# Performance work log

Measured on AMD Instinct MI355X. Metric: run time of the kernel, lower is better.

Reference implementation:

```python
import jax, jax.numpy as jnp
import numpy as np

INF = 1.0e10


def _embed(x, W1, b1, W2, b2):
    # TemplateAngleEmbedder: Linear -> GELU -> Linear
    return jax.nn.gelu(x @ W1 + b1) @ W2 + b2


def setup_inputs() -> dict:
    key = jax.random.key(0)
    ks = jax.random.split(key, 12)
    B, N, K = 2, 768, 30
    d_pair, d_msa, relpos_k = 128, 256, 32
    num_bins = 2 * relpos_k + 1  # 65
    s = 0.02
    # valid rigid frames: random rotations via QR (det fixed to +1) + translations
    A = jax.random.normal(ks[0], (B, N, 3, 3), dtype=jnp.float32)
    Q, _ = jnp.linalg.qr(A)
    Q = Q * jnp.sign(jnp.linalg.det(Q))[..., None, None]
    t = jax.random.normal(ks[1], (B, N, 3), dtype=jnp.float32) * 10.0
    frames = (jnp.zeros((B, N, 4, 4), dtype=jnp.float32)
              .at[..., :3, :3].set(Q)
              .at[..., :3, 3].set(t)
              .at[..., 3, 3].set(1.0))
    residue_index = jnp.tile(jnp.arange(N, dtype=jnp.int32)[None], (B, 1))
    return {
        'tf': jax.random.normal(ks[2], (B, N, 1), dtype=jnp.float32),
        'residue_index': residue_index,
        'true_frame_tensor': frames,
        'seq_mask': jnp.ones((B, N), dtype=jnp.float32),
        'W_tf': jax.random.normal(ks[3], (1, d_msa), dtype=jnp.float32) * s,
        'b_tf': jnp.zeros((d_msa,), dtype=jnp.float32),
        'Wa1': jax.random.normal(ks[4], (5, d_pair), dtype=jnp.float32) * s,
        'ba1': jnp.zeros((d_pair,), dtype=jnp.float32),
        'Wa2': jax.random.normal(ks[5], (d_pair, d_pair), dtype=jnp.float32) * s,
        'ba2': jnp.zeros((d_pair,), dtype=jnp.float32),
        'Wd1': jax.random.normal(ks[6], (3, d_pair), dtype=jnp.float32) * s,
        'bd1': jnp.zeros((d_pair,), dtype=jnp.float32),
        'Wd2': jax.random.normal(ks[7], (d_pair, d_pair), dtype=jnp.float32) * s,
        'bd2': jnp.zeros((d_pair,), dtype=jnp.float32),
        'W_rp': jax.random.normal(ks[8], (num_bins, d_pair), dtype=jnp.float32) * s,
        'b_rp': jnp.zeros((d_pair,), dtype=jnp.float32),
        'topk': 30,
    }


def _pair_features(true_frame_tensor, residue_index, seq_mask, topk):
    # get_pair_info: pairwise dist + masked topk KNN + gather + frame decompose
    B, N = residue_index.shape
    R = true_frame_tensor[..., :3, :3]          # [B,N,3,3]
    t = true_frame_tensor[..., :3, 3]           # [B,N,3]
    xyz = t[:, None, :, :] - t[:, :, None, :]   # [B,i,j,3] = t_j - t_i
    dist = jnp.linalg.norm(xyz, axis=-1)        # [B,N,N]
    eye = jnp.eye(N, dtype=bool)[None]          # [1,N,N]
    smask = seq_mask.astype(bool)
    pair_mask = smask[:, None, :] & smask[:, :, None]
    rel = residue_index[:, None, :] - residue_index[:, :, None]
    connect = jnp.abs(rel) == 1
    d4topk = jnp.where(eye, INF, dist)
    d4topk = jnp.where(pair_mask, d4topk, INF)
    d4topk = jnp.where(connect, -INF, d4topk)
    _, idx = jax.lax.top_k(-d4topk, topk)       # k smallest -> [B,N,K]
    topk_dist = jnp.take_along_axis(dist, idx, axis=-1)          # [B,N,K]
    knn_mask = jnp.take_along_axis(pair_mask & ~eye, idx, axis=-1)
    # gather neighbor frames and decompose into frame i's local coordinates:
    # t_rel = R_i^T (t_j - t_i)
    bidx = jnp.arange(B)[:, None, None]
    tj = t[bidx, idx]                            # [B,N,K,3]
    t_rel = jnp.einsum('bnxy,bnkx->bnky', R, tj - t[:, :, None, :])
    d = topk_dist[..., None]
    direct_angle = jnp.where(d > 0, t_rel / jnp.where(d > 0, d, 1.0), 0.0)
    eye_g = jnp.take_along_axis(jnp.broadcast_to(eye, (B, N, N)), idx, axis=-1)
    conn_g = jnp.take_along_axis(connect, idx, axis=-1)
    f32 = topk_dist.dtype
    ang_in = jnp.concatenate([eye_g[..., None].astype(f32),
                              conn_g[..., None].astype(f32),
                              direct_angle], axis=-1)            # [B,N,K,5]
    dst_in = jnp.concatenate([eye_g[..., None].astype(f32),
                              conn_g[..., None].astype(f32),
                              topk_dist[..., None]], axis=-1)    # [B,N,K,3]
    return ang_in, dst_in, knn_mask


def reference(tf, residue_index, true_frame_tensor, seq_mask,
              W_tf, b_tf, Wa1, ba1, Wa2, ba2, Wd1, bd1, Wd2, bd2,
              W_rp, b_rp, topk):
    relpos_k = (W_rp.shape[0] - 1) // 2
    # pair info computed under no_grad in the original
    ang_in, dst_in, _ = jax.lax.stop_gradient(
        _pair_features(true_frame_tensor, residue_index, seq_mask, topk))
    # tf is replaced by ones in the original forward
    ones_tf = jnp.ones_like(tf[..., :1])
    s = ones_tf @ W_tf + b_tf                                   # [B,N,d_msa]
    pair_rep_angle = _embed(ang_in, Wa1, ba1, Wa2, ba2)         # [B,N,K,d_pair]
    pair_rep_dist = _embed(dst_in, Wd1, bd1, Wd2, bd2)          # [B,N,K,d_pair]
    # relpos embedding (use_chain_relative=False)
    rp = residue_index[:, :, None] - residue_index[:, None, :]
    rp = jnp.clip(rp, -relpos_k, relpos_k) + relpos_k
    oh = jax.nn.one_hot(rp, W_rp.shape[0], dtype=W_rp.dtype)    # [B,N,N,65]
    relpos_emb = oh @ W_rp + b_rp                               # [B,N,N,d_pair]
    return (s, pair_rep_angle, pair_rep_dist, relpos_emb)
```

## Files before the change

### kernel.cpp

```cpp
#include <hip/hip_runtime.h>

typedef unsigned short u16;
typedef unsigned int   u32;
typedef unsigned long long u64;

typedef __attribute__((ext_vector_type(8))) short  short8;
typedef __attribute__((ext_vector_type(4))) float  floatx4;

__device__ __forceinline__ u16 f2bf(float f) {
    u32 u = __float_as_uint(f);
    u32 r = (u + 0x7FFFu + ((u >> 16) & 1u)) >> 16;
    return (u16)r;
}
__device__ __forceinline__ float bfu2f(u16 u) {
    union { u32 i; float f; } v; v.i = ((u32)u) << 16; return v.f;
}

constexpr int N     = 768;
constexpr int TOPK  = 30;
constexpr long OFF_ANG = 393216;
constexpr long OFF_DST = 6291456;
constexpr long OFF_RP  = 12189696;

__device__ __forceinline__ float dist_f32(float dx, float dy, float dz) {
    float s = __fadd_rn(__fadd_rn(__fmul_rn(dx, dx), __fmul_rn(dy, dy)), __fmul_rn(dz, dz));
    return __fsqrt_rn(s);
}

__global__ __launch_bounds__(256) void topk_feat_kernel(
    const float* __restrict__ frames, const int* __restrict__ resi,
    const float* __restrict__ smask, float* __restrict__ feat)
{
    __shared__ float s_t[N * 3];
    __shared__ float s_m[N];
    __shared__ int   s_r[N];
    int tid = threadIdx.x;
    int r0  = blockIdx.x * 4;
    int b   = r0 / N;
    for (int j = tid; j < N; j += 256) {
        s_r[j] = resi[b * N + j];
        s_m[j] = smask[b * N + j];
        long fb = (long)(b * N + j) * 16;
        s_t[j * 3 + 0] = frames[fb + 0 * 4 + 3];
        s_t[j * 3 + 1] = frames[fb + 1 * 4 + 3];
        s_t[j * 3 + 2] = frames[fb + 2 * 4 + 3];
    }
    __syncthreads();

    int wave = tid >> 6, lane = tid & 63;
    int r = r0 + wave;
    int i = r - b * N;
    float ti0 = s_t[i * 3], ti1 = s_t[i * 3 + 1], ti2 = s_t[i * 3 + 2];
    float mi = s_m[i];
    int   ri = s_r[i];

    u64 keys[12];
#pragma unroll
    for (int c = 0; c < 12; c++) {
        int j = lane + 64 * c;
        float dx = __fadd_rn(s_t[j * 3 + 0], -ti0);
        float dy = __fadd_rn(s_t[j * 3 + 1], -ti1);
        float dz = __fadd_rn(s_t[j * 3 + 2], -ti2);
        float dist = dist_f32(dx, dy, dz);
        int rd = s_r[j] - ri;
        bool conn = (rd == 1) || (rd == -1);
        bool bad  = (j == i) || (mi == 0.f) || (s_m[j] == 0.f);
        float d4 = conn ? -1e10f : (bad ? 1e10f : dist);
        u32 u = __float_as_uint(d4);
        u32 su = (u >> 31) ? ~u : (u | 0x80000000u);
        keys[c] = ((u64)su << 32) | (u32)j;
    }

    int my_j = 0;
    for (int k = 0; k < TOPK; k++) {
        u64 m = keys[0];
#pragma unroll
        for (int c = 1; c < 12; c++) m = m < keys[c] ? m : keys[c];
#pragma unroll
        for (int off = 32; off >= 1; off >>= 1) {
            u32 lo = (u32)m, hi = (u32)(m >> 32);
            u32 lo2 = __shfl_xor(lo, off);
            u32 hi2 = __shfl_xor(hi, off);
            u64 o = ((u64)hi2 << 32) | lo2;
            m = m < o ? m : o;
        }
#pragma unroll
        for (int c = 0; c < 12; c++) keys[c] = (keys[c] == m) ? ~0ull : keys[c];
        if (lane == k) my_j = (int)(m & 0xffffffffu);
    }

    if (lane < TOPK) {
        int j = my_j;
        float dx = __fadd_rn(s_t[j * 3 + 0], -ti0);
        float dy = __fadd_rn(s_t[j * 3 + 1], -ti1);
        float dz = __fadd_rn(s_t[j * 3 + 2], -ti2);
        float dist = dist_f32(dx, dy, dz);
        long fb = (long)(b * N + i) * 16;
        float R00 = frames[fb + 0], R01 = frames[fb + 1], R02 = frames[fb + 2];
        float R10 = frames[fb + 4], R11 = frames[fb + 5], R12 = frames[fb + 6];
        float R20 = frames[fb + 8], R21 = frames[fb + 9], R22 = frames[fb + 10];
        float t0 = R00 * dx + R10 * dy + R20 * dz;
        float t1 = R01 * dx + R11 * dy + R21 * dz;
        float t2 = R02 * dx + R12 * dy + R22 * dz;
        float a0 = dist > 0.f ? t0 / dist : 0.f;
        float a1 = dist > 0.f ? t1 / dist : 0.f;
        float a2 = dist > 0.f ? t2 / dist : 0.f;
        int rd = s_r[j] - ri;
        float conn = ((rd == 1) || (rd == -1)) ? 1.f : 0.f;
        float eye  = (j == i) ? 1.f : 0.f;
        long base = ((long)r * TOPK + lane) * 8;
        feat[base + 0] = eye; feat[base + 1] = conn;
        feat[base + 2] = a0;  feat[base + 3] = a1; feat[base + 4] = a2;
        feat[base + 5] = eye; feat[base + 6] = conn; feat[base + 7] = dist;
    }
}

template<int NF, int FOFF>
__device__ __forceinline__ void embed_body3(
    int blk0, const float* __restrict__ feat,
    const float* __restrict__ W1, const float* __restrict__ b1,
    const float* __restrict__ W2, const float* __restrict__ b2,
    float* __restrict__ out,
    u16* s_w2h, u16* s_w2l, float* s_w1, float* s_b1, float* s_b2)
{
    int tid = threadIdx.x;
    for (int e4 = tid; e4 < 4096; e4 += 256) {
        floatx4 w4 = ((const floatx4*)W2)[e4];
        int e  = e4 * 4;
        int kk = e >> 7, nn0 = e & 127;
#pragma unroll
        for (int x = 0; x < 4; x++) {
            float w  = w4[x];
            u16 hi = f2bf(w);
            float lo = __fadd_rn(w, -bfu2f(hi));
            s_w2h[(nn0 + x) * 136 + kk] = hi;
            s_w2l[(nn0 + x) * 136 + kk] = f2bf(lo);
        }
    }
    for (int e = tid; e < NF * 128; e += 256) s_w1[e] = W1[e];
    if (tid < 128) { s_b1[tid] = b1[tid]; s_b2[tid] = b2[tid]; }
    __syncthreads();

    int wave = tid >> 6, lane = tid & 63;
    int m = lane & 15, q = lane >> 4;

#pragma unroll
    for (int tt = 0; tt < 3; tt++) {
        int blk  = blk0 + 240 * tt;
        int row0 = blk * 64 + wave * 16;
        int row  = row0 + m;

        float f[NF];
#pragma unroll
        for (int t = 0; t < NF; t++) f[t] = feat[(long)row * 8 + FOFF + t];

        floatx4 acc[8];
#pragma unroll
        for (int nt = 0; nt < 8; nt++) acc[nt] = (floatx4){0.f, 0.f, 0.f, 0.f};

#pragma unroll
        for (int s = 0; s < 4; s++) {
            short8 ahi, alo;
#pragma unroll
            for (int jj = 0; jj < 8; jj++) {
                int kk = 32 * s + 8 * q + jj;
                float h = s_b1[kk];
#pragma unroll
                for (int t = 0; t < NF; t++) h += f[t] * s_w1[t * 128 + kk];
                float u  = 0.7978845608028654f * (h + 0.044715f * h * h * h);
                float e2 = __expf(-2.f * fabsf(u));
                float th = (1.f - e2) / (1.f + e2);
                th = u < 0.f ? -th : th;
                float g = 0.5f * h * (1.f + th);
                u16 ghi = f2bf(g);
                float glo = __fadd_rn(g, -bfu2f(ghi));
                ahi[jj] = (short)ghi;
                alo[jj] = (short)f2bf(glo);
            }
#pragma unroll
            for (int nt = 0; nt < 8; nt++) {
                int boff = (nt * 16 + m) * 136 + 32 * s + 8 * q;
                short8 bh = *(const short8*)&s_w2h[boff];
                short8 bl = *(const short8*)&s_w2l[boff];
                acc[nt] = __builtin_amdgcn_mfma_f32_16x16x32_bf16(ahi, bh, acc[nt], 0, 0, 0);
                acc[nt] = __builtin_amdgcn_mfma_f32_16x16x32_bf16(alo, bh, acc[nt], 0, 0, 0);
                acc[nt] = __builtin_amdgcn_mfma_f32_16x16x32_bf16(ahi, bl, acc[nt], 0, 0, 0);
            }
        }

#pragma unroll
        for (int nt = 0; nt < 8; nt++) {
#pragma unroll
            for (int rg = 0; rg < 4; rg++) {
                int rr = row0 + q * 4 + rg;
                int cc = nt * 16 + m;
                out[(long)rr * 128 + cc] = acc[nt][rg] + s_b2[cc];
            }
        }
    }
}

__global__ __launch_bounds__(256) void mega_kernel(
    const int* __restrict__ resi,
    const float* __restrict__ W_rp, const float* __restrict__ b_rp,
    const float* __restrict__ feat,
    const float* __restrict__ Wa1, const float* __restrict__ ba1,
    const float* __restrict__ Wa2, const float* __restrict__ ba2,
    const float* __restrict__ Wd1, const float* __restrict__ bd1,
    const float* __restrict__ Wd2, const float* __restrict__ bd2,
    const float* __restrict__ W_tf, const float* __restrict__ b_tf,
    float* __restrict__ out)
{
    __shared__ __align__(16) char smem_raw[73216];
    int tid = threadIdx.x;
    unsigned bx = blockIdx.x;

    if (bx < 1152) {
        float* T   = (float*)smem_raw;
        int*   s_r = (int*)(T + 65 * 128);

        int blk = bx;
        int b   = blk >= 576;

        for (int e = tid; e < 65 * 128; e += 256) T[e] = W_rp[e] + b_rp[e & 127];
        for (int j = tid; j < N; j += 256) s_r[j] = resi[b * N + j];
        __syncthreads();

        long vbase   = (long)blk << 15;
        int  rowbase = (blk - b * 576) << 10;
        floatx4* dst = (floatx4*)(out + OFF_RP) + vbase;

#pragma unroll 4
        for (int it = 0; it < 128; ++it) {
            int lv  = (it << 8) + tid;
            unsigned lrow = (unsigned)(rowbase + (lv >> 5));
            int seg = lv & 31;
            unsigned i = lrow / 768u;
            unsigned j = lrow - i * 768u;
            int d = s_r[i] - s_r[j];
            d = d < -32 ? -32 : (d > 32 ? 32 : d);
            dst[lv] = ((const floatx4*)(T + (unsigned)(d + 32) * 128))[seg];
        }
    } else if (bx < 1632) {
        u16*   s_w2h = (u16*)smem_raw;
        u16*   s_w2l = (u16*)(smem_raw + 34816);
        float* s_w1  = (float*)(smem_raw + 69632);
        float* s_b1  = (float*)(smem_raw + 72192);
        float* s_b2  = (float*)(smem_raw + 72704);
        unsigned eb = bx - 1152;
        if (eb < 240) {
            embed_body3<5, 0>(eb, feat, Wa1, ba1, Wa2, ba2, out + OFF_ANG,
                              s_w2h, s_w2l, s_w1, s_b1, s_b2);
        } else {
            embed_body3<3, 5>(eb - 240, feat, Wd1, bd1, Wd2, bd2, out + OFF_DST,
                              s_w2h, s_w2l, s_w1, s_b1, s_b2);
        }
    } else {
        int gid = (bx - 1632) * 256 + tid;
        int c0  = (gid * 4) & 255;
        floatx4 o;
        o.x = W_tf[c0 + 0] + b_tf[c0 + 0];
        o.y = W_tf[c0 + 1] + b_tf[c0 + 1];
        o.z = W_tf[c0 + 2] + b_tf[c0 + 2];
        o.w = W_tf[c0 + 3] + b_tf[c0 + 3];
        *((floatx4*)out + gid) = o;
    }
}

extern "C" void kernel_launch(void* const* d_in, const int* in_sizes, int n_in,
                              void* d_out, int out_size, void* d_ws, size_t ws_size,
                              hipStream_t stream) {
    const int*   resi   = (const int*)d_in[1];
    const float* frames = (const float*)d_in[2];
    const float* smask  = (const float*)d_in[3];
    const float* W_tf   = (const float*)d_in[4];
    const float* b_tf   = (const float*)d_in[5];
    const float* Wa1    = (const float*)d_in[6];
    const float* ba1    = (const float*)d_in[7];
    const float* Wa2    = (const float*)d_in[8];
    const float* ba2    = (const float*)d_in[9];
    const float* Wd1    = (const float*)d_in[10];
    const float* bd1    = (const float*)d_in[11];
    const float* Wd2    = (const float*)d_in[12];
    const float* bd2    = (const float*)d_in[13];
    const float* W_rp   = (const float*)d_in[14];
    const float* b_rp   = (const float*)d_in[15];
    float* out  = (float*)d_out;
    float* feat = (float*)d_ws;

    hipLaunchKernelGGL(topk_feat_kernel, dim3(384), dim3(256), 0, stream,
                       frames, resi, smask, feat);
    hipLaunchKernelGGL(mega_kernel, dim3(2016), dim3(256), 0, stream,
                       resi, W_rp, b_rp, feat,
                       Wa1, ba1, Wa2, ba2, Wd1, bd1, Wd2, bd2,
                       W_tf, b_tf, out);
}
```

Measured before the change: 747.5 us.

## Pre-split W2 into bf16 hi/lo in global memory and shrink mega-kernel LDS

The bf16 hi/lo split and transpose of the second-layer weights moves out of every embed block into two extra blocks of the top-k kernel, which write it to workspace. Embed blocks now read those B fragments straight from global/L2 instead of LDS, and each block handles one 64-row tile instead of three. Shared memory drops to the relpos table size and launch bounds ask for 4 blocks per CU, which should raise occupancy for the memory-bound relpos writes. The cost is repeated global loads of the weight fragments inside the MFMA loop and more embed blocks that each reload W1 and biases.

```diff
diff --git a/kernel.cpp b/kernel.cpp
--- a/kernel.cpp
+++ b/kernel.cpp
@@ -27,14 +27,37 @@
     return __fsqrt_rn(s);
 }
 
-__global__ __launch_bounds__(256) void topk_feat_kernel(
+__global__ __launch_bounds__(256) void topk_feat_split_kernel(
     const float* __restrict__ frames, const int* __restrict__ resi,
-    const float* __restrict__ smask, float* __restrict__ feat)
+    const float* __restrict__ smask,
+    const float* __restrict__ Wa2, const float* __restrict__ Wd2,
+    float* __restrict__ feat, u16* __restrict__ w2sp)
 {
     __shared__ float s_t[N * 3];
     __shared__ float s_m[N];
     __shared__ int   s_r[N];
     int tid = threadIdx.x;
+
+    if (blockIdx.x >= 384) {
+        const float* W2 = (blockIdx.x == 384) ? Wa2 : Wd2;
+        u16* h = w2sp + (blockIdx.x - 384) * 32768;
+        u16* l = h + 16384;
+        for (int e4 = tid; e4 < 4096; e4 += 256) {
+            floatx4 w4 = ((const floatx4*)W2)[e4];
+            int e  = e4 * 4;
+            int kk = e >> 7, nn0 = e & 127;
+#pragma unroll
+            for (int x = 0; x < 4; x++) {
+                float w  = w4[x];
+                u16 hi = f2bf(w);
+                float lo = __fadd_rn(w, -bfu2f(hi));
+                h[(nn0 + x) * 128 + kk] = hi;
+                l[(nn0 + x) * 128 + kk] = f2bf(lo);
+            }
+        }
+        return;
+    }
+
     int r0  = blockIdx.x * 4;
     int b   = r0 / N;
     for (int j = tid; j < N; j += 256) {
@@ -116,102 +139,85 @@
 }
 
 template<int NF, int FOFF>
-__device__ __forceinline__ void embed_body3(
-    int blk0, const float* __restrict__ feat,
+__device__ __forceinline__ void embed_g(
+    int blk, const float* __restrict__ feat,
     const float* __restrict__ W1, const float* __restrict__ b1,
-    const float* __restrict__ W2, const float* __restrict__ b2,
+    const u16* __restrict__ w2h, const u16* __restrict__ w2l,
+    const float* __restrict__ b2,
     float* __restrict__ out,
-    u16* s_w2h, u16* s_w2l, float* s_w1, float* s_b1, float* s_b2)
+    float* s_w1, float* s_b1, float* s_b2)
 {
     int tid = threadIdx.x;
-    for (int e4 = tid; e4 < 4096; e4 += 256) {
-        floatx4 w4 = ((const floatx4*)W2)[e4];
-        int e  = e4 * 4;
-        int kk = e >> 7, nn0 = e & 127;
-#pragma unroll
-        for (int x = 0; x < 4; x++) {
-            float w  = w4[x];
-            u16 hi = f2bf(w);
-            float lo = __fadd_rn(w, -bfu2f(hi));
-            s_w2h[(nn0 + x) * 136 + kk] = hi;
-            s_w2l[(nn0 + x) * 136 + kk] = f2bf(lo);
-        }
-    }
     for (int e = tid; e < NF * 128; e += 256) s_w1[e] = W1[e];
     if (tid < 128) { s_b1[tid] = b1[tid]; s_b2[tid] = b2[tid]; }
     __syncthreads();
 
     int wave = tid >> 6, lane = tid & 63;
     int m = lane & 15, q = lane >> 4;
-
-#pragma unroll
-    for (int tt = 0; tt < 3; tt++) {
-        int blk  = blk0 + 240 * tt;
-        int row0 = blk * 64 + wave * 16;
-        int row  = row0 + m;
-
-        float f[NF];
-#pragma unroll
-        for (int t = 0; t < NF; t++) f[t] = feat[(long)row * 8 + FOFF + t];
-
-        floatx4 acc[8];
-#pragma unroll
-        for (int nt = 0; nt < 8; nt++) acc[nt] = (floatx4){0.f, 0.f, 0.f, 0.f};
-
-#pragma unroll
-        for (int s = 0; s < 4; s++) {
-            short8 ahi, alo;
-#pragma unroll
-            for (int jj = 0; jj < 8; jj++) {
-                int kk = 32 * s + 8 * q + jj;
-                float h = s_b1[kk];
-#pragma unroll
-                for (int t = 0; t < NF; t++) h += f[t] * s_w1[t * 128 + kk];
-                float u  = 0.7978845608028654f * (h + 0.044715f * h * h * h);
-                float e2 = __expf(-2.f * fabsf(u));
-                float th = (1.f - e2) / (1.f + e2);
-                th = u < 0.f ? -th : th;
-                float g = 0.5f * h * (1.f + th);
-                u16 ghi = f2bf(g);
-                float glo = __fadd_rn(g, -bfu2f(ghi));
-                ahi[jj] = (short)ghi;
-                alo[jj] = (short)f2bf(glo);
-            }
-#pragma unroll
-            for (int nt = 0; nt < 8; nt++) {
-                int boff = (nt * 16 + m) * 136 + 32 * s + 8 * q;
-                short8 bh = *(const short8*)&s_w2h[boff];
-                short8 bl = *(const short8*)&s_w2l[boff];
-                acc[nt] = __builtin_amdgcn_mfma_f32_16x16x32_bf16(ahi, bh, acc[nt], 0, 0, 0);
-                acc[nt] = __builtin_amdgcn_mfma_f32_16x16x32_bf16(alo, bh, acc[nt], 0, 0, 0);
-                acc[nt] = __builtin_amdgcn_mfma_f32_16x16x32_bf16(ahi, bl, acc[nt], 0, 0, 0);
-            }
-        }
-
+    int row0 = blk * 64 + wave * 16;
+    int row  = row0 + m;
+
+    float f[NF];
+#pragma unroll
+    for (int t = 0; t < NF; t++) f[t] = feat[(long)row * 8 + FOFF + t];
+
+    floatx4 acc[8];
+#pragma unroll
+    for (int nt = 0; nt < 8; nt++) acc[nt] = (floatx4){0.f, 0.f, 0.f, 0.f};
+
+#pragma unroll
+    for (int s = 0; s < 4; s++) {
+        short8 ahi, alo;
+#pragma unroll
+        for (int jj = 0; jj < 8; jj++) {
+            int kk = 32 * s + 8 * q + jj;
+            float h = s_b1[kk];
+#pragma unroll
+            for (int t = 0; t < NF; t++) h += f[t] * s_w1[t * 128 + kk];
+            float u  = 0.7978845608028654f * (h + 0.044715f * h * h * h);
+            float e2 = __expf(-2.f * fabsf(u));
+            float th = (1.f - e2) / (1.f + e2);
+            th = u < 0.f ? -th : th;
+            float g = 0.5f * h * (1.f + th);
+            u16 ghi = f2bf(g);
+            float glo = __fadd_rn(g, -bfu2f(ghi));
+            ahi[jj] = (short)ghi;
+            alo[jj] = (short)f2bf(glo);
+        }
 #pragma unroll
         for (int nt = 0; nt < 8; nt++) {
-#pragma unroll
-            for (int rg = 0; rg < 4; rg++) {
-                int rr = row0 + q * 4 + rg;
-                int cc = nt * 16 + m;
-                out[(long)rr * 128 + cc] = acc[nt][rg] + s_b2[cc];
-            }
-        }
-    }
-}
-
-__global__ __launch_bounds__(256) void mega_kernel(
+            int boff = (nt * 16 + m) * 128 + 32 * s + 8 * q;
+            short8 bh = *(const short8*)&w2h[boff];
+            short8 bl = *(const short8*)&w2l[boff];
+            acc[nt] = __builtin_amdgcn_mfma_f32_16x16x32_bf16(ahi, bh, acc[nt], 0, 0, 0);
+            acc[nt] = __builtin_amdgcn_mfma_f32_16x16x32_bf16(alo, bh, acc[nt], 0, 0, 0);
+            acc[nt] = __builtin_amdgcn_mfma_f32_16x16x32_bf16(ahi, bl, acc[nt], 0, 0, 0);
+        }
+    }
+
+#pragma unroll
+    for (int nt = 0; nt < 8; nt++) {
+#pragma unroll
+        for (int rg = 0; rg < 4; rg++) {
+            int rr = row0 + q * 4 + rg;
+            int cc = nt * 16 + m;
+            out[(long)rr * 128 + cc] = acc[nt][rg] + s_b2[cc];
+        }
+    }
+}
+
+__global__ __launch_bounds__(256, 4) void mega_kernel(
     const int* __restrict__ resi,
     const float* __restrict__ W_rp, const float* __restrict__ b_rp,
-    const float* __restrict__ feat,
+    const float* __restrict__ feat, const u16* __restrict__ w2sp,
     const float* __restrict__ Wa1, const float* __restrict__ ba1,
-    const float* __restrict__ Wa2, const float* __restrict__ ba2,
+    const float* __restrict__ ba2,
     const float* __restrict__ Wd1, const float* __restrict__ bd1,
-    const float* __restrict__ Wd2, const float* __restrict__ bd2,
+    const float* __restrict__ bd2,
     const float* __restrict__ W_tf, const float* __restrict__ b_tf,
     float* __restrict__ out)
 {
-    __shared__ __align__(16) char smem_raw[73216];
+    __shared__ __align__(16) char smem_raw[65 * 128 * 4 + N * 4];
     int tid = threadIdx.x;
     unsigned bx = blockIdx.x;
 
@@ -241,22 +247,22 @@
             d = d < -32 ? -32 : (d > 32 ? 32 : d);
             dst[lv] = ((const floatx4*)(T + (unsigned)(d + 32) * 128))[seg];
         }
-    } else if (bx < 1632) {
-        u16*   s_w2h = (u16*)smem_raw;
-        u16*   s_w2l = (u16*)(smem_raw + 34816);
-        float* s_w1  = (float*)(smem_raw + 69632);
-        float* s_b1  = (float*)(smem_raw + 72192);
-        float* s_b2  = (float*)(smem_raw + 72704);
+    } else if (bx < 2592) {
+        float* s_w1 = (float*)smem_raw;
+        float* s_b1 = (float*)(smem_raw + 2560);
+        float* s_b2 = (float*)(smem_raw + 3072);
         unsigned eb = bx - 1152;
-        if (eb < 240) {
-            embed_body3<5, 0>(eb, feat, Wa1, ba1, Wa2, ba2, out + OFF_ANG,
-                              s_w2h, s_w2l, s_w1, s_b1, s_b2);
+        if (eb < 720) {
+            embed_g<5, 0>(eb, feat, Wa1, ba1,
+                          w2sp, w2sp + 16384, ba2, out + OFF_ANG,
+                          s_w1, s_b1, s_b2);
         } else {
-            embed_body3<3, 5>(eb - 240, feat, Wd1, bd1, Wd2, bd2, out + OFF_DST,
-                              s_w2h, s_w2l, s_w1, s_b1, s_b2);
+            embed_g<3, 5>(eb - 720, feat, Wd1, bd1,
+                          w2sp + 32768, w2sp + 49152, bd2, out + OFF_DST,
+                          s_w1, s_b1, s_b2);
         }
     } else {
-        int gid = (bx - 1632) * 256 + tid;
+        int gid = (bx - 2592) * 256 + tid;
         int c0  = (gid * 4) & 255;
         floatx4 o;
         o.x = W_tf[c0 + 0] + b_tf[c0 + 0];
@@ -287,11 +293,12 @@
     const float* b_rp   = (const float*)d_in[15];
     float* out  = (float*)d_out;
     float* feat = (float*)d_ws;
-
-    hipLaunchKernelGGL(topk_feat_kernel, dim3(384), dim3(256), 0, stream,
-                       frames, resi, smask, feat);
-    hipLaunchKernelGGL(mega_kernel, dim3(2016), dim3(256), 0, stream,
-                       resi, W_rp, b_rp, feat,
-                       Wa1, ba1, Wa2, ba2, Wd1, bd1, Wd2, bd2,
+    u16*   w2sp = (u16*)((char*)d_ws + 46080l * 8 * 4);
+
+    hipLaunchKernelGGL(topk_feat_split_kernel, dim3(386), dim3(256), 0, stream,
+                       frames, resi, smask, Wa2, Wd2, feat, w2sp);
+    hipLaunchKernelGGL(mega_kernel, dim3(2976), dim3(256), 0, stream,
+                       resi, W_rp, b_rp, feat, w2sp,
+                       Wa1, ba1, ba2, Wd1, bd1, bd2,
                        W_tf, b_tf, out);
 }
```

Result: no change. 734.3 us (-1.8%).
